# Kernel optimization log

Hardware: AMD Instinct MI355X
Metric: run time of the kernel (lower is better)

## Reference

```python
import jax, jax.numpy as jnp
import numpy as np

B, L, DX, H = 2, 2048, 1024, 16
DQ = DK = DV = DR = 64


def setup_inputs() -> dict:
    key0 = jax.random.key(0)
    ks = jax.random.split(key0, 14)
    def lin(kw, kb, din, dout):
        s = 1.0 / np.sqrt(din)
        w = jax.random.uniform(kw, (din, dout), jnp.float32, -s, s)
        b = jax.random.uniform(kb, (dout,), jnp.float32, -s, s)
        return w, b
    value = jax.random.normal(ks[0], (B, L, DX), jnp.float32)
    key_t = jax.random.normal(ks[1], (B, L, DX), jnp.float32)
    query = jax.random.normal(ks[2], (B, L, DX), jnp.float32)
    mask = jnp.tril(jnp.ones((L, L), jnp.int32))[None, None]  # [1,1,L,L] causal
    Wq_w, Wq_b = lin(ks[3], ks[4], DX, DQ * H)
    Wk_w, Wk_b = lin(ks[5], ks[6], DX, DK * H)
    Wv_w, Wv_b = lin(ks[7], ks[8], DX, DV * H)
    Wr_w, Wr_b = lin(ks[9], ks[10], DX, DR * H)
    wo_w, wo_b = lin(ks[11], ks[12], DV * H, DX)
    return dict(value=value, key=key_t, query=query, mask=mask,
                Wq_w=Wq_w, Wq_b=Wq_b, Wk_w=Wk_w, Wk_b=Wk_b,
                Wv_w=Wv_w, Wv_b=Wv_b, Wr_w=Wr_w, Wr_b=Wr_b,
                wo_w=wo_w, wo_b=wo_b)


def reference(value, key, query, mask, Wq_w, Wq_b, Wk_w, Wk_b, Wv_w, Wv_b,
              Wr_w, Wr_b, wo_w, wo_b):
    N, Lq, _ = query.shape
    q = (query @ Wq_w + Wq_b).reshape(N, Lq, H, DQ)   # nqhd
    k = (key @ Wk_w + Wk_b).reshape(N, -1, H, DK)     # nkhd
    v = (value @ Wv_w + Wv_b).reshape(N, -1, H, DV)   # nlhd
    r = (query @ Wr_w + Wr_b).reshape(N, Lq, H, DR)   # computed but unused (as in source)
    del r
    scores = jnp.einsum('nqhd,nkhd->nhqk', q, k)      # [N,H,L,L] materialized
    scores = jnp.where(mask == 0, jnp.float32(-1e20), scores)
    scale = jnp.float32(np.sqrt(DX))  # source divides by embedding_size**0.5
    attn = jax.nn.softmax(scores / scale, axis=3)
    out = jnp.einsum('nhql,nlhd->nqhd', attn, v).reshape(N, Lq, H * DV)
    return out @ wo_w + wo_b
```

## Files before the change

kernel.cpp:

```cpp
#include <hip/hip_runtime.h>
#include <hip/hip_bf16.h>
#include <type_traits>

typedef __hip_bfloat16 bf16;
typedef __attribute__((ext_vector_type(4))) float f32x4;
typedef __attribute__((ext_vector_type(8))) short s16x8;

#define DEVINL __device__ __forceinline__

#if defined(__has_builtin) && __has_builtin(__builtin_amdgcn_exp2f)
#define FEXP2(x) __builtin_amdgcn_exp2f(x)
#else
#define FEXP2(x) __exp2f(x)
#endif

DEVINL s16x8 load16B(const void* p) {
  s16x8 v;
  __builtin_memcpy(&v, __builtin_assume_aligned(p, 16), 16);
  return v;
}
DEVINL void store16B(void* p, s16x8 v) {
  __builtin_memcpy(__builtin_assume_aligned(p, 16), &v, 16);
}
DEVINL s16x8 cvt8(const float* p) {
  f32x4 a, b;
  __builtin_memcpy(&a, __builtin_assume_aligned(p, 16), 16);
  __builtin_memcpy(&b, __builtin_assume_aligned(p + 4, 16), 16);
  union { s16x8 v; bf16 h[8]; } u;
#pragma unroll
  for (int i = 0; i < 4; i++) {
    u.h[i] = __float2bfloat16(a[i]);
    u.h[4 + i] = __float2bfloat16(b[i]);
  }
  return u.v;
}
DEVINL void gload_lds16(const bf16* g, bf16* l) {
  __builtin_amdgcn_global_load_lds(
      (__attribute__((address_space(1))) void*)(void*)const_cast<bf16*>(g),
      (__attribute__((address_space(3))) void*)l, 16, 0, 0);
}

static constexpr int SEQ = 2048;
#define QSCALE 0.04508422002778011f

__global__ __launch_bounds__(256) void k_transpose(
    const float* __restrict__ Wq, const float* __restrict__ Wk,
    const float* __restrict__ Wv, const float* __restrict__ Wo,
    bf16* __restrict__ dst) {
  __shared__ float t[64][65];
  const float* src = blockIdx.z == 0 ? Wq : blockIdx.z == 1 ? Wk
                   : blockIdx.z == 2 ? Wv : Wo;
  bf16* out = dst + (size_t)blockIdx.z * 1024 * 1024;
  const int r0 = blockIdx.y * 64, c0 = blockIdx.x * 64;
#pragma unroll
  for (int i = 0; i < 16; i++) {
    int e = i * 256 + threadIdx.x;
    int r = e >> 6, c = e & 63;
    t[r][c] = src[(size_t)(r0 + r) * 1024 + c0 + c];
  }
  __syncthreads();
#pragma unroll
  for (int i = 0; i < 16; i++) {
    int e = i * 256 + threadIdx.x;
    int r = e >> 6, c = e & 63;
    out[(size_t)(c0 + r) * 1024 + r0 + c] = __float2bfloat16(t[c][r]);
  }
}

__global__ __launch_bounds__(256) void k_cvt3(
    const float* __restrict__ q, const float* __restrict__ k,
    const float* __restrict__ v, bf16* __restrict__ dstbase) {
  const float* src = blockIdx.z == 0 ? q : blockIdx.z == 1 ? k : v;
  bf16* dst = dstbase + (size_t)blockIdx.z * 4194304;
  size_t i = ((size_t)blockIdx.x * 256 + threadIdx.x) * 8;
  store16B(dst + i, cvt8(src + i));
}

template <typename XT>
DEVINL void gemm_core(const XT* __restrict__ X, const bf16* __restrict__ WT,
                      const float* __restrict__ bias, void* __restrict__ dstv,
                      const int mode, const float scale, const int m0,
                      const int n0) {
  __shared__ alignas(16) bf16 As[128 * 32];
  __shared__ alignas(16) bf16 Bs[128 * 32];
  const int tid = threadIdx.x;
  const int w = tid >> 6, lane = tid & 63, lg = lane >> 4, li = lane & 15;
  const int wm = w >> 1, wn = w & 1;

  f32x4 acc[4][4] = {};

  for (int kt = 0; kt < 32; ++kt) {
    const int k0 = kt * 32;
#pragma unroll
    for (int j = 0; j < 2; j++) {
      const int cb = (j * 4 + w) * 64;
      const int c = cb + lane;
      const int r = c >> 2, kk = (c & 3) * 8;
      gload_lds16(WT + (size_t)(n0 + r) * 1024 + k0 + kk, Bs + cb * 8);
      if constexpr (std::is_same_v<XT, bf16>)
        gload_lds16(X + (size_t)(m0 + r) * 1024 + k0 + kk, As + cb * 8);
    }
    if constexpr (std::is_same_v<XT, float>) {
#pragma unroll
      for (int j = 0; j < 2; j++) {
        const int c = j * 256 + tid;
        const int r = c >> 2, kk = (c & 3) * 8;
        s16x8 a = cvt8(X + (size_t)(m0 + r) * 1024 + k0 + kk);
        store16B((char*)As + c * 16, a);
      }
    }
    __syncthreads();
    s16x8 af[4], bfv[4];
#pragma unroll
    for (int i = 0; i < 4; i++)
      af[i] = load16B((char*)As + (wm * 64 + i * 16 + li) * 64 + lg * 16);
#pragma unroll
    for (int j = 0; j < 4; j++)
      bfv[j] = load16B((char*)Bs + (wn * 64 + j * 16 + li) * 64 + lg * 16);
#pragma unroll
    for (int i = 0; i < 4; i++)
#pragma unroll
      for (int j = 0; j < 4; j++)
        acc[i][j] = __builtin_amdgcn_mfma_f32_16x16x32_bf16(af[i], bfv[j],
                                                            acc[i][j], 0, 0, 0);
    __syncthreads();
  }

#pragma unroll
  for (int j = 0; j < 4; j++) {
    const int n = n0 + wn * 64 + j * 16 + li;
    const float bv = bias[n];
#pragma unroll
    for (int i = 0; i < 4; i++) {
      const int mrow = m0 + wm * 64 + i * 16 + lg * 4;
      f32x4 a = acc[i][j];
      if (mode == 2) {
        float* dst = (float*)dstv;
#pragma unroll
        for (int r = 0; r < 4; r++)
          dst[(size_t)(mrow + r) * 1024 + n] = a[r] + bv;
      } else if (mode == 0) {
        bf16* dst = (bf16*)dstv;
#pragma unroll
        for (int r = 0; r < 4; r++) {
          int m = mrow + r;
          size_t idx =
              ((size_t)((m >> 11) * 16 + (n >> 6)) * SEQ + (m & 2047)) * 64 +
              (n & 63);
          dst[idx] = __float2bfloat16((a[r] + bv) * scale);
        }
      } else {
        bf16* dst = (bf16*)dstv;
        size_t base =
            ((size_t)((mrow >> 11) * 16 + (n >> 6)) * 64 + (n & 63)) * SEQ +
            (mrow & 2047);
        bf16 tmp[4];
#pragma unroll
        for (int r = 0; r < 4; r++) tmp[r] = __float2bfloat16(a[r] + bv);
        __builtin_memcpy(__builtin_assume_aligned(dst + base, 8), tmp, 8);
      }
    }
  }
}

__global__ __launch_bounds__(256) void k_gemm_qkv_bf16(
    const bf16* __restrict__ xbase, const bf16* __restrict__ WTbase,
    const float* __restrict__ qb, const float* __restrict__ kb,
    const float* __restrict__ vb, bf16* __restrict__ qo,
    bf16* __restrict__ ko, bf16* __restrict__ vto) {
  const int z = blockIdx.z;
  const bf16* X = xbase + (size_t)z * 4194304;
  const bf16* WT = WTbase + (size_t)z * 1048576;
  const float* bias = z == 0 ? qb : z == 1 ? kb : vb;
  void* dst = z == 0 ? (void*)qo : z == 1 ? (void*)ko : (void*)vto;
  gemm_core<bf16>(X, WT, bias, dst, z == 2 ? 1 : 0, z == 0 ? QSCALE : 1.0f,
                  blockIdx.x * 128, blockIdx.y * 128);
}

__global__ __launch_bounds__(256) void k_gemm_qkv_f32(
    const float* __restrict__ qx, const float* __restrict__ kx,
    const float* __restrict__ vx, const bf16* __restrict__ WTbase,
    const float* __restrict__ qb, const float* __restrict__ kb,
    const float* __restrict__ vb, bf16* __restrict__ qo,
    bf16* __restrict__ ko, bf16* __restrict__ vto) {
  const int z = blockIdx.z;
  const float* X = z == 0 ? qx : z == 1 ? kx : vx;
  const bf16* WT = WTbase + (size_t)z * 1048576;
  const float* bias = z == 0 ? qb : z == 1 ? kb : vb;
  void* dst = z == 0 ? (void*)qo : z == 1 ? (void*)ko : (void*)vto;
  gemm_core<float>(X, WT, bias, dst, z == 2 ? 1 : 0, z == 0 ? QSCALE : 1.0f,
                   blockIdx.x * 128, blockIdx.y * 128);
}

__global__ __launch_bounds__(256) void k_gemm_out(
    const bf16* __restrict__ X, const bf16* __restrict__ WT,
    const float* __restrict__ bias, float* __restrict__ out) {
  gemm_core<bf16>(X, WT, bias, out, 2, 1.0f, blockIdx.x * 128,
                  blockIdx.y * 128);
}

__global__ __launch_bounds__(256) void k_attn(
    const bf16* __restrict__ qb, const bf16* __restrict__ kb,
    const bf16* __restrict__ vtb, bf16* __restrict__ attn) {
  __shared__ alignas(16) bf16 Ks[2][64 * 64];
  __shared__ alignas(16) bf16 Vts[2][64 * 64];
  __shared__ alignas(16) bf16 Ps[4][16 * 72];
  const int tid = threadIdx.x;
  const int w = tid >> 6, lane = tid & 63, lg = lane >> 4, li = lane & 15;
  const int bh = blockIdx.x;
  const int qblk = 31 - blockIdx.y;
  const int qrow = qblk * 64 + w * 16;
  const bf16* qh = qb + (size_t)bh * SEQ * 64;
  const bf16* kh = kb + (size_t)bh * SEQ * 64;
  const bf16* vth = vtb + (size_t)bh * 64 * SEQ;

  s16x8 aq[2];
#pragma unroll
  for (int c = 0; c < 2; c++)
    aq[c] = load16B(qh + (size_t)(qrow + li) * 64 + c * 32 + lg * 8);

  f32x4 o[4] = {};
  float m_run = -1e38f;
  float l_run = 0.f;

  const int c0s = tid, c1s = 256 + tid;
  const int by0 = (c0s * 16) ^ (((c0s >> 3) & 7) << 4);
  const int by1 = (c1s * 16) ^ (((c1s >> 3) & 7) << 4);
  const int d0 = c0s >> 3, kk0 = (c0s & 7) * 8;
  const int d1 = c1s >> 3, kk1 = (c1s & 7) * 8;

  s16x8 rk[2], rv[2];
  rk[0] = load16B(kh + (size_t)c0s * 8);
  rk[1] = load16B(kh + (size_t)c1s * 8);
  rv[0] = load16B(vth + (size_t)d0 * SEQ + kk0);
  rv[1] = load16B(vth + (size_t)d1 * SEQ + kk1);
  store16B((char*)Ks[0] + by0, rk[0]);
  store16B((char*)Ks[0] + by1, rk[1]);
  store16B((char*)Vts[0] + by0, rv[0]);
  store16B((char*)Vts[0] + by1, rv[1]);
  if (qblk >= 1) {
    rk[0] = load16B(kh + (size_t)64 * 64 + c0s * 8);
    rk[1] = load16B(kh + (size_t)64 * 64 + c1s * 8);
    rv[0] = load16B(vth + (size_t)d0 * SEQ + 64 + kk0);
    rv[1] = load16B(vth + (size_t)d1 * SEQ + 64 + kk1);
  }
  __syncthreads();

  for (int kbk = 0; kbk <= qblk; ++kbk) {
    const int cur = kbk & 1;
    if (kbk < qblk) {
      store16B((char*)Ks[cur ^ 1] + by0, rk[0]);
      store16B((char*)Ks[cur ^ 1] + by1, rk[1]);
      store16B((char*)Vts[cur ^ 1] + by0, rv[0]);
      store16B((char*)Vts[cur ^ 1] + by1, rv[1]);
      if (kbk + 2 <= qblk) {
        const int kn = (kbk + 2) * 64;
        rk[0] = load16B(kh + (size_t)kn * 64 + c0s * 8);
        rk[1] = load16B(kh + (size_t)kn * 64 + c1s * 8);
        rv[0] = load16B(vth + (size_t)d0 * SEQ + kn + kk0);
        rv[1] = load16B(vth + (size_t)d1 * SEQ + kn + kk1);
      }
    }

    f32x4 s[4];
    __builtin_amdgcn_s_setprio(1);
#pragma unroll
    for (int t = 0; t < 4; t++) {
      f32x4 z = {};
#pragma unroll
      for (int c = 0; c < 2; c++) {
        int row = t * 16 + li;
        s16x8 ak = load16B((char*)Ks[cur] +
                           ((row * 128 + c * 64 + lg * 16) ^ ((row & 7) << 4)));
        z = __builtin_amdgcn_mfma_f32_16x16x32_bf16(ak, aq[c], z, 0, 0, 0);
      }
      s[t] = z;
    }
    __builtin_amdgcn_s_setprio(0);

    if (kbk == qblk) {
      const int kb0 = kbk * 64 + lg * 4;
      const int qg = qrow + li;
#pragma unroll
      for (int t = 0; t < 4; t++)
#pragma unroll
        for (int r = 0; r < 4; r++)
          if (kb0 + t * 16 + r > qg) s[t][r] = -1e30f;
    }

    f32x4 mm = s[0];
#pragma unroll
    for (int t = 1; t < 4; t++)
#pragma unroll
      for (int r = 0; r < 4; r++) mm[r] = fmaxf(mm[r], s[t][r]);
    float mr = fmaxf(fmaxf(mm[0], mm[1]), fmaxf(mm[2], mm[3]));
    mr = fmaxf(mr, __shfl_xor(mr, 16));
    mr = fmaxf(mr, __shfl_xor(mr, 32));

    const bool grow = !__all(mr <= m_run + 8.0f);
    const float mn = grow ? fmaxf(m_run, mr) : m_run;

    float p[4][4];
    float s0 = 0.f, s1 = 0.f, s2 = 0.f, s3 = 0.f;
#pragma unroll
    for (int r = 0; r < 4; r++) {
      float p0 = FEXP2(s[0][r] - mn), p1 = FEXP2(s[1][r] - mn);
      float p2 = FEXP2(s[2][r] - mn), p3 = FEXP2(s[3][r] - mn);
      p[0][r] = p0; p[1][r] = p1; p[2][r] = p2; p[3][r] = p3;
      s0 += p0; s1 += p1; s2 += p2; s3 += p3;
    }
    float sum = (s0 + s1) + (s2 + s3);
    sum += __shfl_xor(sum, 16);
    sum += __shfl_xor(sum, 32);

    if (grow) {
      const float cr = FEXP2(m_run - mn);
      l_run = l_run * cr + sum;
      m_run = mn;
      const int sb = (lane & 48);
      float crr[4];
#pragma unroll
      for (int r = 0; r < 4; r++) crr[r] = __shfl(cr, sb + (sb >> 2) + r);
#pragma unroll
      for (int t = 0; t < 4; t++)
#pragma unroll
        for (int r = 0; r < 4; r++) o[t][r] *= crr[r];
    } else {
      l_run += sum;
    }

#pragma unroll
    for (int t = 0; t < 4; t++) {
      bf16 tmp[4];
#pragma unroll
      for (int r = 0; r < 4; r++) tmp[r] = __float2bfloat16(p[t][r]);
      __builtin_memcpy(
          __builtin_assume_aligned(&Ps[w][li * 72 + t * 16 + lg * 4], 8), tmp,
          8);
    }

    s16x8 ap[2];
#pragma unroll
    for (int c = 0; c < 2; c++)
      ap[c] = load16B(&Ps[w][li * 72 + c * 32 + lg * 8]);

    __builtin_amdgcn_s_setprio(1);
#pragma unroll
    for (int t = 0; t < 4; t++) {
#pragma unroll
      for (int c = 0; c < 2; c++) {
        int row = t * 16 + li;
        s16x8 bv = load16B((char*)Vts[cur] +
                           ((row * 128 + c * 64 + lg * 16) ^ ((row & 7) << 4)));
        o[t] = __builtin_amdgcn_mfma_f32_16x16x32_bf16(ap[c], bv, o[t], 0, 0, 0);
      }
    }
    __builtin_amdgcn_s_setprio(0);
    __syncthreads();
  }

  const int b = bh >> 4, h = bh & 15;
  const float inv = 1.0f / l_run;
  const int sb = (lane & 48);
  float invr[4];
#pragma unroll
  for (int r = 0; r < 4; r++) invr[r] = __shfl(inv, sb + (sb >> 2) + r);
#pragma unroll
  for (int r = 0; r < 4; r++)
#pragma unroll
    for (int t = 0; t < 4; t++) {
      size_t idx = (size_t)(b * SEQ + qrow + lg * 4 + r) * 1024 + h * 64 +
                   t * 16 + li;
      attn[idx] = __float2bfloat16(o[t][r] * invr[r]);
    }
}

extern "C" void kernel_launch(void* const* d_in, const int* in_sizes, int n_in,
                              void* d_out, int out_size, void* d_ws,
                              size_t ws_size, hipStream_t stream) {
  (void)in_sizes; (void)n_in; (void)out_size;
  const float* value = (const float*)d_in[0];
  const float* key   = (const float*)d_in[1];
  const float* query = (const float*)d_in[2];
  const float* Wq_w = (const float*)d_in[4];
  const float* Wq_b = (const float*)d_in[5];
  const float* Wk_w = (const float*)d_in[6];
  const float* Wk_b = (const float*)d_in[7];
  const float* Wv_w = (const float*)d_in[8];
  const float* Wv_b = (const float*)d_in[9];
  const float* wo_w = (const float*)d_in[12];
  const float* wo_b = (const float*)d_in[13];

  bf16* ws = (bf16*)d_ws;
  const size_t MM = 1048576;
  bf16* WT = ws;

  k_transpose<<<dim3(16, 16, 4), 256, 0, stream>>>(Wq_w, Wk_w, Wv_w, wo_w, WT);

  if (ws_size >= 28ull * MM * 2) {
    bf16* xbuf = ws + 4 * MM;
    bf16* qbuf = ws + 16 * MM;
    bf16* kbuf = ws + 20 * MM;
    bf16* vtbf = ws + 24 * MM;
    bf16* abuf = ws + 4 * MM;
    k_cvt3<<<dim3(2048, 1, 3), 256, 0, stream>>>(query, key, value, xbuf);
    k_gemm_qkv_bf16<<<dim3(32, 8, 3), 256, 0, stream>>>(
        xbuf, WT, Wq_b, Wk_b, Wv_b, qbuf, kbuf, vtbf);
    k_attn<<<dim3(32, 32), 256, 0, stream>>>(qbuf, kbuf, vtbf, abuf);
    k_gemm_out<<<dim3(32, 8), 256, 0, stream>>>(abuf, WT + 3 * MM, wo_b,
                                                (float*)d_out);
  } else {
    bf16* qbuf = ws + 4 * MM;
    bf16* kbuf = ws + 8 * MM;
    bf16* vtbf = ws + 12 * MM;
    bf16* abuf = ws + 16 * MM;
    k_gemm_qkv_f32<<<dim3(32, 8, 3), 256, 0, stream>>>(
        query, key, value, WT, Wq_b, Wk_b, Wv_b, qbuf, kbuf, vtbf);
    k_attn<<<dim3(32, 32), 256, 0, stream>>>(qbuf, kbuf, vtbf, abuf);
    k_gemm_out<<<dim3(32, 8), 256, 0, stream>>>(abuf, WT + 3 * MM, wo_b,
                                                (float*)d_out);
  }
}
```

Before: 124.1 us.

## Stage V-transpose epilogue through LDS, swizzle P buffer, reorder causal q-blocks

The V projection epilogue now writes bias-added bf16 tiles into a shared-memory transpose buffer, then emits coalesced 16-byte stores along the sequence dimension instead of scattered 8-byte stores. The attention kernel replaces the padded P scratch with an XOR-swizzled layout to avoid bank conflicts. It also remaps blockIdx.y to q-blocks in an interleaved heavy/light order to balance causal work across the dispatch. The transpose buffer adds about 17KB of LDS to every GEMM instantiation, which could reduce occupancy for the Q/K and output GEMMs.

```diff
diff --git a/kernel.cpp b/kernel.cpp
--- a/kernel.cpp
+++ b/kernel.cpp
@@ -83,6 +83,7 @@
                       const int n0) {
   __shared__ alignas(16) bf16 As[128 * 32];
   __shared__ alignas(16) bf16 Bs[128 * 32];
+  __shared__ alignas(16) bf16 T[64][136];
   const int tid = threadIdx.x;
   const int w = tid >> 6, lane = tid & 63, lg = lane >> 4, li = lane & 15;
   const int wm = w >> 1, wn = w & 1;
@@ -126,6 +127,42 @@
     __syncthreads();
   }
 
+  if (mode == 1) {
+    bf16* dst = (bf16*)dstv;
+    const int b = m0 >> 11;
+#pragma unroll
+    for (int p = 0; p < 2; p++) {
+      __syncthreads();
+      if (wn == p) {
+#pragma unroll
+        for (int j = 0; j < 4; j++) {
+          const int nn = j * 16 + li;
+          const float bv = bias[n0 + p * 64 + nn];
+#pragma unroll
+          for (int i = 0; i < 4; i++) {
+            const int mm = wm * 64 + i * 16 + lg * 4;
+            f32x4 a = acc[i][j];
+            bf16 tmp[4];
+#pragma unroll
+            for (int r = 0; r < 4; r++) tmp[r] = __float2bfloat16(a[r] + bv);
+            __builtin_memcpy(__builtin_assume_aligned(&T[nn][mm], 8), tmp, 8);
+          }
+        }
+      }
+      __syncthreads();
+#pragma unroll
+      for (int q = 0; q < 4; q++) {
+        const int chunk = q * 256 + tid;
+        const int row = chunk >> 4, off = (chunk & 15) * 8;
+        s16x8 vv = load16B(&T[row][off]);
+        const int n = n0 + p * 64 + row;
+        size_t base = (((size_t)b * 16 + (n >> 6)) * 64 + (n & 63)) * SEQ +
+                      (m0 & 2047) + off;
+        store16B(dst + base, vv);
+      }
+    }
+    return;
+  }
 #pragma unroll
   for (int j = 0; j < 4; j++) {
     const int n = n0 + wn * 64 + j * 16 + li;
@@ -139,7 +176,7 @@
 #pragma unroll
         for (int r = 0; r < 4; r++)
           dst[(size_t)(mrow + r) * 1024 + n] = a[r] + bv;
-      } else if (mode == 0) {
+      } else {
         bf16* dst = (bf16*)dstv;
 #pragma unroll
         for (int r = 0; r < 4; r++) {
@@ -149,15 +186,6 @@
               (n & 63);
           dst[idx] = __float2bfloat16((a[r] + bv) * scale);
         }
-      } else {
-        bf16* dst = (bf16*)dstv;
-        size_t base =
-            ((size_t)((mrow >> 11) * 16 + (n >> 6)) * 64 + (n & 63)) * SEQ +
-            (mrow & 2047);
-        bf16 tmp[4];
-#pragma unroll
-        for (int r = 0; r < 4; r++) tmp[r] = __float2bfloat16(a[r] + bv);
-        __builtin_memcpy(__builtin_assume_aligned(dst + base, 8), tmp, 8);
       }
     }
   }
@@ -204,11 +232,13 @@
     const bf16* __restrict__ vtb, bf16* __restrict__ attn) {
   __shared__ alignas(16) bf16 Ks[2][64 * 64];
   __shared__ alignas(16) bf16 Vts[2][64 * 64];
-  __shared__ alignas(16) bf16 Ps[4][16 * 72];
+  __shared__ alignas(16) bf16 Ps[4][16 * 64];
   const int tid = threadIdx.x;
   const int w = tid >> 6, lane = tid & 63, lg = lane >> 4, li = lane & 15;
   const int bh = blockIdx.x;
-  const int qblk = 31 - blockIdx.y;
+  const int y = blockIdx.y;
+  const int qblk = (y < 8) ? 31 - y : (y < 16) ? y + 8
+                 : (y < 24) ? 31 - y : y - 24;
   const int qrow = qblk * 64 + w * 16;
   const bf16* qh = qb + (size_t)bh * SEQ * 64;
   const bf16* kh = kb + (size_t)bh * SEQ * 64;
@@ -228,6 +258,7 @@
   const int by1 = (c1s * 16) ^ (((c1s >> 3) & 7) << 4);
   const int d0 = c0s >> 3, kk0 = (c0s & 7) * 8;
   const int d1 = c1s >> 3, kk1 = (c1s & 7) * 8;
+  const int psw = (li & 7) << 3;
 
   s16x8 rk[2], rv[2];
   rk[0] = load16B(kh + (size_t)c0s * 8);
@@ -335,14 +366,15 @@
 #pragma unroll
       for (int r = 0; r < 4; r++) tmp[r] = __float2bfloat16(p[t][r]);
       __builtin_memcpy(
-          __builtin_assume_aligned(&Ps[w][li * 72 + t * 16 + lg * 4], 8), tmp,
-          8);
+          __builtin_assume_aligned(
+              &Ps[w][li * 64 + ((t * 16 + lg * 4) ^ psw)], 8),
+          tmp, 8);
     }
 
     s16x8 ap[2];
 #pragma unroll
     for (int c = 0; c < 2; c++)
-      ap[c] = load16B(&Ps[w][li * 72 + c * 32 + lg * 8]);
+      ap[c] = load16B(&Ps[w][li * 64 + ((c * 32 + lg * 8) ^ psw)]);
 
     __builtin_amdgcn_s_setprio(1);
 #pragma unroll
```

After: 134.2 us. 8.1% more time.

## Vectorize GEMM epilogue stores, swizzle P tile, and rebalance causal attention block order

Applied to the files above, without the earlier changes.

The GEMM core is now templated on output mode. For the Q/K and output projections the MFMA operands are swapped so each lane holds four consecutive columns, which lets the epilogue use 16-byte fp32 stores and 8-byte bf16 stores with a vectorized bias load instead of scattered scalar stores. The attention kernel's P scratch buffer drops its padding in favour of an XOR swizzle. The causal query-block ordering is also interleaved so that long and short blocks are mixed across dispatch waves. These changes target uncoalesced epilogue writes and tail imbalance, at the cost of more complex indexing.

```diff
diff --git a/kernel.cpp b/kernel.cpp
--- a/kernel.cpp
+++ b/kernel.cpp
@@ -76,13 +76,11 @@
   store16B(dst + i, cvt8(src + i));
 }
 
-template <typename XT>
-DEVINL void gemm_core(const XT* __restrict__ X, const bf16* __restrict__ WT,
+template <typename XT, int MODE>
+DEVINL void gemm_body(const XT* __restrict__ X, const bf16* __restrict__ WT,
                       const float* __restrict__ bias, void* __restrict__ dstv,
-                      const int mode, const float scale, const int m0,
-                      const int n0) {
-  __shared__ alignas(16) bf16 As[128 * 32];
-  __shared__ alignas(16) bf16 Bs[128 * 32];
+                      const float scale, const int m0, const int n0,
+                      bf16* As, bf16* Bs) {
   const int tid = threadIdx.x;
   const int w = tid >> 6, lane = tid & 63, lg = lane >> 4, li = lane & 15;
   const int wm = w >> 1, wn = w & 1;
@@ -120,44 +118,67 @@
 #pragma unroll
     for (int i = 0; i < 4; i++)
 #pragma unroll
-      for (int j = 0; j < 4; j++)
-        acc[i][j] = __builtin_amdgcn_mfma_f32_16x16x32_bf16(af[i], bfv[j],
-                                                            acc[i][j], 0, 0, 0);
+      for (int j = 0; j < 4; j++) {
+        if constexpr (MODE == 1)
+          acc[i][j] = __builtin_amdgcn_mfma_f32_16x16x32_bf16(
+              af[i], bfv[j], acc[i][j], 0, 0, 0);
+        else
+          acc[i][j] = __builtin_amdgcn_mfma_f32_16x16x32_bf16(
+              bfv[j], af[i], acc[i][j], 0, 0, 0);
+      }
     __syncthreads();
   }
 
-#pragma unroll
-  for (int j = 0; j < 4; j++) {
-    const int n = n0 + wn * 64 + j * 16 + li;
-    const float bv = bias[n];
+  if constexpr (MODE == 1) {
+    bf16* dst = (bf16*)dstv;
+#pragma unroll
+    for (int j = 0; j < 4; j++) {
+      const int n = n0 + wn * 64 + j * 16 + li;
+      const float bv = bias[n];
+#pragma unroll
+      for (int i = 0; i < 4; i++) {
+        const int mrow = m0 + wm * 64 + i * 16 + lg * 4;
+        f32x4 a = acc[i][j];
+        size_t base =
+            (((size_t)(mrow >> 11) * 16 + (n >> 6)) * 64 + (n & 63)) * SEQ +
+            (mrow & 2047);
+        bf16 tmp[4];
+#pragma unroll
+        for (int r = 0; r < 4; r++) tmp[r] = __float2bfloat16(a[r] + bv);
+        __builtin_memcpy(__builtin_assume_aligned(dst + base, 8), tmp, 8);
+      }
+    }
+  } else {
+    f32x4 bias4[4];
+#pragma unroll
+    for (int j = 0; j < 4; j++)
+      __builtin_memcpy(&bias4[j], bias + n0 + wn * 64 + j * 16 + lg * 4, 16);
 #pragma unroll
     for (int i = 0; i < 4; i++) {
-      const int mrow = m0 + wm * 64 + i * 16 + lg * 4;
-      f32x4 a = acc[i][j];
-      if (mode == 2) {
+      const int m = m0 + wm * 64 + i * 16 + li;
+      if constexpr (MODE == 2) {
         float* dst = (float*)dstv;
 #pragma unroll
-        for (int r = 0; r < 4; r++)
-          dst[(size_t)(mrow + r) * 1024 + n] = a[r] + bv;
-      } else if (mode == 0) {
-        bf16* dst = (bf16*)dstv;
-#pragma unroll
-        for (int r = 0; r < 4; r++) {
-          int m = mrow + r;
-          size_t idx =
-              ((size_t)((m >> 11) * 16 + (n >> 6)) * SEQ + (m & 2047)) * 64 +
-              (n & 63);
-          dst[idx] = __float2bfloat16((a[r] + bv) * scale);
+        for (int j = 0; j < 4; j++) {
+          const int nb = n0 + wn * 64 + j * 16 + lg * 4;
+          f32x4 v = acc[i][j] + bias4[j];
+          __builtin_memcpy(__builtin_assume_aligned(
+                               dst + (size_t)m * 1024 + nb, 16), &v, 16);
         }
       } else {
         bf16* dst = (bf16*)dstv;
-        size_t base =
-            ((size_t)((mrow >> 11) * 16 + (n >> 6)) * 64 + (n & 63)) * SEQ +
-            (mrow & 2047);
-        bf16 tmp[4];
-#pragma unroll
-        for (int r = 0; r < 4; r++) tmp[r] = __float2bfloat16(a[r] + bv);
-        __builtin_memcpy(__builtin_assume_aligned(dst + base, 8), tmp, 8);
+        const int l = m & 2047, bb = m >> 11;
+#pragma unroll
+        for (int j = 0; j < 4; j++) {
+          const int nb = n0 + wn * 64 + j * 16 + lg * 4;
+          bf16 tmp[4];
+#pragma unroll
+          for (int r = 0; r < 4; r++)
+            tmp[r] = __float2bfloat16((acc[i][j][r] + bias4[j][r]) * scale);
+          size_t idx = (((size_t)bb * 16 + (nb >> 6)) * SEQ + l) * 64 +
+                       (nb & 63);
+          __builtin_memcpy(__builtin_assume_aligned(dst + idx, 8), tmp, 8);
+        }
       }
     }
   }
@@ -168,13 +189,19 @@
     const float* __restrict__ qb, const float* __restrict__ kb,
     const float* __restrict__ vb, bf16* __restrict__ qo,
     bf16* __restrict__ ko, bf16* __restrict__ vto) {
+  __shared__ alignas(16) bf16 As[128 * 32];
+  __shared__ alignas(16) bf16 Bs[128 * 32];
   const int z = blockIdx.z;
   const bf16* X = xbase + (size_t)z * 4194304;
   const bf16* WT = WTbase + (size_t)z * 1048576;
   const float* bias = z == 0 ? qb : z == 1 ? kb : vb;
-  void* dst = z == 0 ? (void*)qo : z == 1 ? (void*)ko : (void*)vto;
-  gemm_core<bf16>(X, WT, bias, dst, z == 2 ? 1 : 0, z == 0 ? QSCALE : 1.0f,
-                  blockIdx.x * 128, blockIdx.y * 128);
+  if (z == 2)
+    gemm_body<bf16, 1>(X, WT, bias, (void*)vto, 1.0f, blockIdx.x * 128,
+                       blockIdx.y * 128, As, Bs);
+  else
+    gemm_body<bf16, 0>(X, WT, bias, z == 0 ? (void*)qo : (void*)ko,
+                       z == 0 ? QSCALE : 1.0f, blockIdx.x * 128,
+                       blockIdx.y * 128, As, Bs);
 }
 
 __global__ __launch_bounds__(256) void k_gemm_qkv_f32(
@@ -183,20 +210,28 @@
     const float* __restrict__ qb, const float* __restrict__ kb,
     const float* __restrict__ vb, bf16* __restrict__ qo,
     bf16* __restrict__ ko, bf16* __restrict__ vto) {
+  __shared__ alignas(16) bf16 As[128 * 32];
+  __shared__ alignas(16) bf16 Bs[128 * 32];
   const int z = blockIdx.z;
   const float* X = z == 0 ? qx : z == 1 ? kx : vx;
   const bf16* WT = WTbase + (size_t)z * 1048576;
   const float* bias = z == 0 ? qb : z == 1 ? kb : vb;
-  void* dst = z == 0 ? (void*)qo : z == 1 ? (void*)ko : (void*)vto;
-  gemm_core<float>(X, WT, bias, dst, z == 2 ? 1 : 0, z == 0 ? QSCALE : 1.0f,
-                   blockIdx.x * 128, blockIdx.y * 128);
+  if (z == 2)
+    gemm_body<float, 1>(X, WT, bias, (void*)vto, 1.0f, blockIdx.x * 128,
+                        blockIdx.y * 128, As, Bs);
+  else
+    gemm_body<float, 0>(X, WT, bias, z == 0 ? (void*)qo : (void*)ko,
+                        z == 0 ? QSCALE : 1.0f, blockIdx.x * 128,
+                        blockIdx.y * 128, As, Bs);
 }
 
 __global__ __launch_bounds__(256) void k_gemm_out(
     const bf16* __restrict__ X, const bf16* __restrict__ WT,
     const float* __restrict__ bias, float* __restrict__ out) {
-  gemm_core<bf16>(X, WT, bias, out, 2, 1.0f, blockIdx.x * 128,
-                  blockIdx.y * 128);
+  __shared__ alignas(16) bf16 As[128 * 32];
+  __shared__ alignas(16) bf16 Bs[128 * 32];
+  gemm_body<bf16, 2>(X, WT, bias, (void*)out, 1.0f, blockIdx.x * 128,
+                     blockIdx.y * 128, As, Bs);
 }
 
 __global__ __launch_bounds__(256) void k_attn(
@@ -204,11 +239,13 @@
     const bf16* __restrict__ vtb, bf16* __restrict__ attn) {
   __shared__ alignas(16) bf16 Ks[2][64 * 64];
   __shared__ alignas(16) bf16 Vts[2][64 * 64];
-  __shared__ alignas(16) bf16 Ps[4][16 * 72];
+  __shared__ alignas(16) bf16 Ps[4][16 * 64];
   const int tid = threadIdx.x;
   const int w = tid >> 6, lane = tid & 63, lg = lane >> 4, li = lane & 15;
   const int bh = blockIdx.x;
-  const int qblk = 31 - blockIdx.y;
+  const int y = blockIdx.y;
+  const int qblk = (y < 8) ? 31 - y : (y < 16) ? y + 8
+                 : (y < 24) ? 31 - y : y - 24;
   const int qrow = qblk * 64 + w * 16;
   const bf16* qh = qb + (size_t)bh * SEQ * 64;
   const bf16* kh = kb + (size_t)bh * SEQ * 64;
@@ -228,6 +265,7 @@
   const int by1 = (c1s * 16) ^ (((c1s >> 3) & 7) << 4);
   const int d0 = c0s >> 3, kk0 = (c0s & 7) * 8;
   const int d1 = c1s >> 3, kk1 = (c1s & 7) * 8;
+  const int psw = (li & 7) << 3;
 
   s16x8 rk[2], rv[2];
   rk[0] = load16B(kh + (size_t)c0s * 8);
@@ -335,14 +373,15 @@
 #pragma unroll
       for (int r = 0; r < 4; r++) tmp[r] = __float2bfloat16(p[t][r]);
       __builtin_memcpy(
-          __builtin_assume_aligned(&Ps[w][li * 72 + t * 16 + lg * 4], 8), tmp,
-          8);
+          __builtin_assume_aligned(
+              &Ps[w][li * 64 + ((t * 16 + lg * 4) ^ psw)], 8),
+          tmp, 8);
     }
 
     s16x8 ap[2];
 #pragma unroll
     for (int c = 0; c < 2; c++)
-      ap[c] = load16B(&Ps[w][li * 72 + c * 32 + lg * 8]);
+      ap[c] = load16B(&Ps[w][li * 64 + ((c * 32 + lg * 8) ^ psw)]);
 
     __builtin_amdgcn_s_setprio(1);
 #pragma unroll
```

Measured after the change: 127.5 us. 2.7% more time.
